# Performance work log

Hardware: AMD Instinct MI355X
Metric: run time of the kernel (lower is better)

Reference implementation:

```python
import jax, jax.numpy as jnp
import numpy as np

N_NODES = 30000
N_EDGES = 480000
IN_CH, NF, OUT_CH = 64, 128, 3
N_HIDDEN = 6  # GCN(num_layers=7): conv0 (in->nf) + 6 convs (nf->nf)
SLOPE = 0.02


def setup_inputs() -> dict:
    key = jax.random.key(0)
    ks = jax.random.split(key, 8)
    x = jax.random.normal(ks[0], (N_NODES, IN_CH), dtype=jnp.float32)
    edge_index = jax.random.randint(ks[1], (2, N_EDGES), 0, N_NODES, dtype=jnp.int64)
    W0 = jax.random.normal(ks[2], (IN_CH, NF), dtype=jnp.float32) * (1.0 / np.sqrt(IN_CH))
    b0 = jnp.zeros((NF,), dtype=jnp.float32)
    Wh = jax.random.normal(ks[3], (N_HIDDEN, NF, NF), dtype=jnp.float32) * (1.0 / np.sqrt(NF))
    bh = jnp.zeros((N_HIDDEN, NF), dtype=jnp.float32)
    Wout = jax.random.normal(ks[4], (NF, OUT_CH), dtype=jnp.float32) * (1.0 / np.sqrt(NF))
    bout = jnp.zeros((OUT_CH,), dtype=jnp.float32)
    return {"x": x, "edge_index": edge_index, "W0": W0, "b0": b0,
            "Wh": Wh, "bh": bh, "Wout": Wout, "bout": bout}


def _gcn_norm(edge_index, n):
    # PyG GCNConv default: add self-loops, symmetric normalization D^-1/2 (A+I) D^-1/2
    loop = jnp.arange(n, dtype=edge_index.dtype)
    src = jnp.concatenate([edge_index[0], loop])
    dst = jnp.concatenate([edge_index[1], loop])
    deg = jax.ops.segment_sum(jnp.ones_like(dst, dtype=jnp.float32), dst, num_segments=n)
    dinv = jax.lax.rsqrt(deg)  # deg >= 1 due to self-loops
    norm = dinv[src] * dinv[dst]  # [E+N]
    return src, dst, norm


def _gcn_conv(h, W, b, src, dst, norm, n):
    h = h @ W                                   # [N, F_out]
    msg = h[src] * norm[:, None]                # gather + scale  [E+N, F_out]
    out = jax.ops.segment_sum(msg, dst, num_segments=n)  # scatter-add
    return out + b


def reference(x, edge_index, W0, b0, Wh, bh, Wout, bout):
    n = x.shape[0]
    src, dst, norm = _gcn_norm(edge_index, n)
    # 7-layer GCN stack with LeakyReLU(0.02) between layers; dropout is
    # identity in eval mode (training=False).
    h = _gcn_conv(x, W0, b0, src, dst, norm, n)
    for i in range(N_HIDDEN):
        h = jax.nn.leaky_relu(h, SLOPE)
        h = _gcn_conv(h, Wh[i], bh[i], src, dst, norm, n)
    # outer forward: leaky_relu -> dropout(eval=identity) -> out conv -> tanh*0.5
    h = jax.nn.leaky_relu(h, SLOPE)
    h = _gcn_conv(h, Wout, bout, src, dst, norm, n)
    return jnp.tanh(h) * 0.5
```

## Files before the change

kernel.cpp:

```cpp
#include <hip/hip_runtime.h>
#include <hip/hip_fp16.h>
#include <math.h>

#define NN 30000
#define NE 480000
#define NB 118
#define INVSCALE (1.0f / 4096.0f)

typedef _Float16 half8 __attribute__((ext_vector_type(8)));
typedef float floatx4 __attribute__((ext_vector_type(4)));
typedef float floatx2 __attribute__((ext_vector_type(2)));

__device__ __forceinline__ float lrelu(float v) { return v > 0.0f ? v : v * 0.02f; }

__device__ __forceinline__ float4 fma4(float4 v, float w, float4 a) {
    a.x = fmaf(v.x, w, a.x);
    a.y = fmaf(v.y, w, a.y);
    a.z = fmaf(v.z, w, a.z);
    a.w = fmaf(v.w, w, a.w);
    return a;
}

__device__ __forceinline__ float4 loadh4(const __half* p) {
    uint2 raw = *(const uint2*)p;
    float2 f0 = __half22float2(*(__half2*)&raw.x);
    float2 f1 = __half22float2(*(__half2*)&raw.y);
    return make_float4(f0.x, f0.y, f1.x, f1.y);
}

__device__ __forceinline__ void loadf8x8(const unsigned char* p, float4* lo, float4* hi) {
    uint2 raw = *(const uint2*)p;
    floatx2 a = __builtin_amdgcn_cvt_pk_f32_fp8(raw.x, false);
    floatx2 b = __builtin_amdgcn_cvt_pk_f32_fp8(raw.x, true);
    floatx2 c = __builtin_amdgcn_cvt_pk_f32_fp8(raw.y, false);
    floatx2 d = __builtin_amdgcn_cvt_pk_f32_fp8(raw.y, true);
    *lo = make_float4(a.x, a.y, b.x, b.y);
    *hi = make_float4(c.x, c.y, d.x, d.y);
}

__device__ __forceinline__ void stnt_f8(unsigned char* p, float v) {
    int pk = __builtin_amdgcn_cvt_pk_fp8_f32(v, v, 0, false);
    __builtin_nontemporal_store((unsigned char)pk, p);
}


__global__ void k_count(const int* __restrict__ ei, int* __restrict__ cnt,
                        const float* __restrict__ W0, const float* __restrict__ Wh,
                        const float* __restrict__ b0, const float* __restrict__ bh,
                        const float* __restrict__ x,
                        __half* __restrict__ W0t, __half* __restrict__ Wht,
                        float* __restrict__ bs, __half* __restrict__ x16) {
    int g = blockIdx.x * 256 + threadIdx.x;
    if (g < NE) atomicAdd(&cnt[ei[NE + g]], 1);
    {
        float4 v = *(const float4*)&x[(size_t)g * 4];
        __half2 a = __floats2half2_rn(v.x, v.y);
        __half2 b = __floats2half2_rn(v.z, v.w);
        uint2 pk;
        pk.x = *(unsigned int*)&a;
        pk.y = *(unsigned int*)&b;
        *(uint2*)&x16[(size_t)g * 4] = pk;
    }
    if (g < 8192) {
        int k = g >> 7, n = g & 127;
        W0t[n * 64 + k] = __float2half(W0[g] * 64.0f);
    } else if (g < 8192 + 98304) {
        int j = g - 8192;
        int l = j >> 14;
        int r = j & 16383;
        int k = r >> 7, n = r & 127;
        Wht[l * 16384 + n * 128 + k] = __float2half(Wh[j] * 2.0f);
    } else if (g < 8192 + 98304 + 896) {
        int j = g - 8192 - 98304;
        float sc;
        if (j < 128) sc = 64.0f;
        else sc = (float)(1 << (7 + ((j - 128) >> 7)));
        bs[j] = (j < 128 ? b0[j] : bh[j - 128]) * sc;
    }
}

__global__ void k_scan1(const int* __restrict__ cnt, int* __restrict__ bsum,
                        float* __restrict__ dinv) {
    __shared__ int sd[256];
    int tid = threadIdx.x;
    int i = blockIdx.x * 256 + tid;
    int v = (i < NN) ? cnt[i] : 0;
    if (i < NN) dinv[i] = 1.0f / sqrtf((float)(v + 1));
    sd[tid] = v;
    __syncthreads();
    for (int off = 128; off > 0; off >>= 1) {
        if (tid < off) sd[tid] += sd[tid + off];
        __syncthreads();
    }
    if (tid == 0) bsum[blockIdx.x] = sd[0];
}

__global__ void k_scan3(const int* __restrict__ cnt, const int* __restrict__ bsum,
                        int* __restrict__ row_ptr, int* __restrict__ cursor) {
    __shared__ int sd[256];
    __shared__ int offs[128];
    int tid = threadIdx.x;
    if (tid < 128) offs[tid] = (tid < blockIdx.x) ? bsum[tid] : 0;
    __syncthreads();
    for (int o = 64; o > 0; o >>= 1) {
        if (tid < o) offs[tid] += offs[tid + o];
        __syncthreads();
    }
    int i = blockIdx.x * 256 + tid;
    int v = (i < NN) ? cnt[i] : 0;
    sd[tid] = v;
    __syncthreads();
    for (int off = 1; off < 256; off <<= 1) {
        int t = (tid >= off) ? sd[tid - off] : 0;
        __syncthreads();
        sd[tid] += t;
        __syncthreads();
    }
    if (i < NN) {
        int excl = offs[0] + sd[tid] - v;
        row_ptr[i] = excl;
        cursor[i] = excl;
        if (i == NN - 1) row_ptr[NN] = excl + v;
    }
}

__global__ void k_fill(const int* __restrict__ ei, const float* __restrict__ dinv,
                       int* __restrict__ cursor, int2* __restrict__ csr) {
    int e = blockIdx.x * 256 + threadIdx.x;
    if (e < NE) {
        int s = ei[e];
        int d = ei[NE + e];
        int pos = atomicAdd(&cursor[d], 1);
        float w = dinv[s] * dinv[d];
        csr[pos] = make_int2(s, __float_as_int(w));
    }
}


__launch_bounds__(256)
__global__ void k_layer0(const __half* __restrict__ x, const int* __restrict__ row_ptr,
                         const int2* __restrict__ csr, const float* __restrict__ dinv,
                         const __half* __restrict__ Wt, const float* __restrict__ bias,
                         unsigned char* __restrict__ out8) {
    __shared__ _Float16 hsF[2 * 4 * 16 * 8];
    int tid = threadIdx.x;
    int node0 = blockIdx.x * 16;
    {
        int nl = tid >> 4;
        int node = node0 + nl;
        int c = (tid & 15) * 4;
        float di = dinv[node];
        float w0 = di * di;
        float4 hv = loadh4(&x[(size_t)node * 64 + c]);
        float4 acc[8];
        acc[0] = make_float4(hv.x * w0, hv.y * w0, hv.z * w0, hv.w * w0);
        #pragma unroll
        for (int j = 1; j < 8; j++) acc[j] = make_float4(0.f, 0.f, 0.f, 0.f);
        int e = row_ptr[node];
        int e1 = row_ptr[node + 1];
        for (; e + 8 <= e1; e += 8) {
            int2 sw[8];
            #pragma unroll
            for (int j = 0; j < 8; j++) sw[j] = csr[e + j];
            float4 v[8];
            #pragma unroll
            for (int j = 0; j < 8; j++) v[j] = loadh4(&x[(size_t)sw[j].x * 64 + c]);
            #pragma unroll
            for (int j = 0; j < 8; j++) acc[j] = fma4(v[j], __int_as_float(sw[j].y), acc[j]);
        }
        for (; e < e1; ++e) {
            int2 sw = csr[e];
            float4 v = loadh4(&x[(size_t)sw.x * 64 + c]);
            acc[0] = fma4(v, __int_as_float(sw.y), acc[0]);
        }
        #pragma unroll
        for (int j = 1; j < 8; j++) {
            acc[0].x += acc[j].x;
            acc[0].y += acc[j].y;
            acc[0].z += acc[j].z;
            acc[0].w += acc[j].w;
        }
        int ks = c >> 5, quad = (c >> 3) & 3, jj = c & 7;
        __half2 p0 = __floats2half2_rn(acc[0].x, acc[0].y);
        __half2 p1 = __floats2half2_rn(acc[0].z, acc[0].w);
        uint2 pk;
        pk.x = *(unsigned int*)&p0;
        pk.y = *(unsigned int*)&p1;
        *(uint2*)&hsF[((ks * 4 + quad) * 16 + nl) * 8 + jj] = pk;
    }
    __syncthreads();
    int wave = tid >> 6, lane = tid & 63, quad = lane >> 4, ln = lane & 15;
    half8 afrag[2];
    #pragma unroll
    for (int ks = 0; ks < 2; ks++)
        afrag[ks] = *(const half8*)&hsF[((ks * 4 + quad) * 16 + ln) * 8];
    #pragma unroll
    for (int tc = 0; tc < 2; tc++) {
        int tt = wave + tc * 4;
        floatx4 acc = (floatx4){0.f, 0.f, 0.f, 0.f};
        #pragma unroll
        for (int ks = 0; ks < 2; ks++) {
            half8 b = *(const half8*)&Wt[(size_t)(tt * 16 + ln) * 64 + ks * 32 + quad * 8];
            acc = __builtin_amdgcn_mfma_f32_16x16x32_f16(afrag[ks], b, acc, 0, 0, 0);
        }
        int col = tt * 16 + ln;
        float bb = bias[col];
        #pragma unroll
        for (int r = 0; r < 4; r++) {
            int row = node0 + quad * 4 + r;
            stnt_f8(&out8[(size_t)row * 128 + col], lrelu(acc[r] + bb));
        }
    }
}

template <bool LAST>
__launch_bounds__(256)
__global__ void k_layer_h(const unsigned char* __restrict__ h, const int* __restrict__ row_ptr,
                          const int2* __restrict__ csr, const float* __restrict__ dinv,
                          const __half* __restrict__ Wt, const float* __restrict__ bias,
                          unsigned char* __restrict__ out8, const float* __restrict__ Wout,
                          float* __restrict__ u) {
    __shared__ _Float16 hsF[4 * 4 * 16 * 8];
    __shared__ float uacc[4][16][3];
    int tid = threadIdx.x;
    int node0 = blockIdx.x * 16;
    {
        int nl = tid >> 4;
        int node = node0 + nl;
        int c = (tid & 15) * 8;
        float di = dinv[node];
        float w0 = di * di;
        float4 hlo, hhi;
        loadf8x8(&h[(size_t)node * 128 + c], &hlo, &hhi);
        float4 acc[4][2];
        acc[0][0] = make_float4(hlo.x * w0, hlo.y * w0, hlo.z * w0, hlo.w * w0);
        acc[0][1] = make_float4(hhi.x * w0, hhi.y * w0, hhi.z * w0, hhi.w * w0);
        #pragma unroll
        for (int j = 1; j < 4; j++) {
            acc[j][0] = make_float4(0.f, 0.f, 0.f, 0.f);
            acc[j][1] = make_float4(0.f, 0.f, 0.f, 0.f);
        }
        int e = row_ptr[node];
        int e1 = row_ptr[node + 1];
        for (; e + 4 <= e1; e += 4) {
            int2 sw[4];
            #pragma unroll
            for (int j = 0; j < 4; j++) sw[j] = csr[e + j];
            float4 vlo[4], vhi[4];
            #pragma unroll
            for (int j = 0; j < 4; j++)
                loadf8x8(&h[(size_t)sw[j].x * 128 + c], &vlo[j], &vhi[j]);
            #pragma unroll
            for (int j = 0; j < 4; j++) {
                float w = __int_as_float(sw[j].y);
                acc[j][0] = fma4(vlo[j], w, acc[j][0]);
                acc[j][1] = fma4(vhi[j], w, acc[j][1]);
            }
        }
        for (; e < e1; ++e) {
            int2 sw = csr[e];
            float4 vlo, vhi;
            loadf8x8(&h[(size_t)sw.x * 128 + c], &vlo, &vhi);
            float w = __int_as_float(sw.y);
            acc[0][0] = fma4(vlo, w, acc[0][0]);
            acc[0][1] = fma4(vhi, w, acc[0][1]);
        }
        #pragma unroll
        for (int j = 1; j < 4; j++) {
            acc[0][0].x += acc[j][0].x; acc[0][0].y += acc[j][0].y;
            acc[0][0].z += acc[j][0].z; acc[0][0].w += acc[j][0].w;
            acc[0][1].x += acc[j][1].x; acc[0][1].y += acc[j][1].y;
            acc[0][1].z += acc[j][1].z; acc[0][1].w += acc[j][1].w;
        }
        int ks = c >> 5, quad = (c >> 3) & 3;
        __half2 p0 = __floats2half2_rn(acc[0][0].x, acc[0][0].y);
        __half2 p1 = __floats2half2_rn(acc[0][0].z, acc[0][0].w);
        __half2 p2 = __floats2half2_rn(acc[0][1].x, acc[0][1].y);
        __half2 p3 = __floats2half2_rn(acc[0][1].z, acc[0][1].w);
        uint4 pk;
        pk.x = *(unsigned int*)&p0;
        pk.y = *(unsigned int*)&p1;
        pk.z = *(unsigned int*)&p2;
        pk.w = *(unsigned int*)&p3;
        *(uint4*)&hsF[((ks * 4 + quad) * 16 + nl) * 8] = pk;
    }
    __syncthreads();
    int wave = tid >> 6, lane = tid & 63, quad = lane >> 4, ln = lane & 15;
    half8 afrag[4];
    #pragma unroll
    for (int ks = 0; ks < 4; ks++)
        afrag[ks] = *(const half8*)&hsF[((ks * 4 + quad) * 16 + ln) * 8];

    float up[4][3];
    if (LAST) {
        #pragma unroll
        for (int r = 0; r < 4; r++)
            #pragma unroll
            for (int cc = 0; cc < 3; cc++) up[r][cc] = 0.f;
    }

    #pragma unroll
    for (int tc = 0; tc < 2; tc++) {
        int tt = wave + tc * 4;
        floatx4 acc = (floatx4){0.f, 0.f, 0.f, 0.f};
        #pragma unroll
        for (int ks = 0; ks < 4; ks++) {
            half8 b = *(const half8*)&Wt[(size_t)(tt * 16 + ln) * 128 + ks * 32 + quad * 8];
            acc = __builtin_amdgcn_mfma_f32_16x16x32_f16(afrag[ks], b, acc, 0, 0, 0);
        }
        int col = tt * 16 + ln;
        float bb = bias[col];
        if (LAST) {
            float w0o = Wout[col * 3 + 0];
            float w1o = Wout[col * 3 + 1];
            float w2o = Wout[col * 3 + 2];
            #pragma unroll
            for (int r = 0; r < 4; r++) {
                float hv = lrelu(acc[r] + bb);
                up[r][0] = fmaf(hv, w0o, up[r][0]);
                up[r][1] = fmaf(hv, w1o, up[r][1]);
                up[r][2] = fmaf(hv, w2o, up[r][2]);
            }
        } else {
            #pragma unroll
            for (int r = 0; r < 4; r++) {
                int row = node0 + quad * 4 + r;
                stnt_f8(&out8[(size_t)row * 128 + col], lrelu(acc[r] + bb));
            }
        }
    }

    if (LAST) {
        #pragma unroll
        for (int m = 1; m < 16; m <<= 1) {
            #pragma unroll
            for (int r = 0; r < 4; r++) {
                #pragma unroll
                for (int cc = 0; cc < 3; cc++)
                    up[r][cc] += __shfl_xor(up[r][cc], m);
            }
        }
        if (ln == 0) {
            #pragma unroll
            for (int r = 0; r < 4; r++) {
                #pragma unroll
                for (int cc = 0; cc < 3; cc++)
                    uacc[wave][quad * 4 + r][cc] = up[r][cc];
            }
        }
        __syncthreads();
        if (tid < 48) {
            int row = tid / 3, cc = tid % 3;
            float s = (uacc[0][row][cc] + uacc[1][row][cc]) +
                      (uacc[2][row][cc] + uacc[3][row][cc]);
            u[(size_t)(node0 + row) * 3 + cc] = s;
        }
    }
}


__global__ void k_agg_out(const float* __restrict__ u, const int* __restrict__ row_ptr,
                          const int2* __restrict__ csr, const float* __restrict__ dinv,
                          const float* __restrict__ bout, float* __restrict__ out) {
    int node = blockIdx.x * 256 + threadIdx.x;
    if (node >= NN) return;
    float di = dinv[node], w0 = di * di;
    float s0 = u[(size_t)node * 3 + 0] * w0;
    float s1 = u[(size_t)node * 3 + 1] * w0;
    float s2 = u[(size_t)node * 3 + 2] * w0;
    float b0a = 0.f, b1a = 0.f, b2a = 0.f;
    int e = row_ptr[node];
    int e1 = row_ptr[node + 1];
    for (; e + 2 <= e1; e += 2) {
        int2 swa = csr[e], swb = csr[e + 1];
        float wa = __int_as_float(swa.y), wb = __int_as_float(swb.y);
        const float* ua = &u[(size_t)swa.x * 3];
        const float* ub = &u[(size_t)swb.x * 3];
        s0 = fmaf(ua[0], wa, s0);
        s1 = fmaf(ua[1], wa, s1);
        s2 = fmaf(ua[2], wa, s2);
        b0a = fmaf(ub[0], wb, b0a);
        b1a = fmaf(ub[1], wb, b1a);
        b2a = fmaf(ub[2], wb, b2a);
    }
    for (; e < e1; ++e) {
        int2 sw = csr[e];
        float w = __int_as_float(sw.y);
        const float* us = &u[(size_t)sw.x * 3];
        s0 = fmaf(us[0], w, s0);
        s1 = fmaf(us[1], w, s1);
        s2 = fmaf(us[2], w, s2);
    }
    out[(size_t)node * 3 + 0] = tanhf((s0 + b0a) * INVSCALE + bout[0]) * 0.5f;
    out[(size_t)node * 3 + 1] = tanhf((s1 + b1a) * INVSCALE + bout[1]) * 0.5f;
    out[(size_t)node * 3 + 2] = tanhf((s2 + b2a) * INVSCALE + bout[2]) * 0.5f;
}


extern "C" void kernel_launch(void* const* d_in, const int* in_sizes, int n_in,
                              void* d_out, int out_size, void* d_ws, size_t ws_size,
                              hipStream_t stream) {
    const float* x        = (const float*)d_in[0];
    const int*   ei       = (const int*)d_in[1];
    const float* W0       = (const float*)d_in[2];
    const float* b0       = (const float*)d_in[3];
    const float* Wh       = (const float*)d_in[4];
    const float* bh       = (const float*)d_in[5];
    const float* Wout     = (const float*)d_in[6];
    const float* bout     = (const float*)d_in[7];
    float* out            = (float*)d_out;

    char* ws = (char*)d_ws;
    float*  bufA   = (float*)(ws + 0);
    unsigned char* bufB8 = (unsigned char*)(ws + 15360000);
    unsigned char* bufC8 = (unsigned char*)(ws + 23040000);
    __half* x16    = (__half*)(ws + 30720000);
    __half* W0t16  = (__half*)(ws + 34560000);
    __half* Wht16  = (__half*)(ws + 34576384);
    float*  bs     = (float*)(ws + 34772992);
    float*  dinv   = (float*)(ws + 34776576);
    int*    cnt    = (int*)  (ws + 34896576);
    int*    row_ptr= (int*)  (ws + 35016576);
    int*    cursor = (int*)  (ws + 35136640);
    int2*   csr    = (int2*) (ws + 35256640);

    int* bsum = (int*)bufA;

    hipMemsetAsync(cnt, 0, NN * sizeof(int), stream);
    k_count<<<(NE + 255) / 256, 256, 0, stream>>>(ei, cnt, W0, Wh, b0, bh, x,
                                                  W0t16, Wht16, bs, x16);
    k_scan1<<<NB, 256, 0, stream>>>(cnt, bsum, dinv);
    k_scan3<<<NB, 256, 0, stream>>>(cnt, bsum, row_ptr, cursor);
    k_fill<<<(NE + 255) / 256, 256, 0, stream>>>(ei, dinv, cursor, csr);

    k_layer0<<<NN / 16, 256, 0, stream>>>(x16, row_ptr, csr, dinv, W0t16, bs, bufB8);

    unsigned char* hin = bufB8;
    unsigned char* hout = bufC8;
    for (int i = 0; i < 5; i++) {
        k_layer_h<false><<<NN / 16, 256, 0, stream>>>(hin, row_ptr, csr, dinv,
                                                      Wht16 + (size_t)i * 16384,
                                                      bs + 128 + (size_t)i * 128, hout,
                                                      Wout, bufA);
        unsigned char* t = hin; hin = hout; hout = t;
    }
    k_layer_h<true><<<NN / 16, 256, 0, stream>>>(hin, row_ptr, csr, dinv,
                                                 Wht16 + (size_t)5 * 16384,
                                                 bs + 128 + (size_t)5 * 128, hout,
                                                 Wout, bufA );

    k_agg_out<<<(NN + 255) / 256, 256, 0, stream>>>(bufA, row_ptr, csr, dinv, bout, out);
}
```

Before: 297.5 us.

## Fuse all GCN stages into a persistent megakernel with grid barriers

Replaces the sequence of count, scan, fill, per-layer and output kernels with one persistent kernel of 256 blocks x 512 threads that steps through the stages using a software grid barrier on atomics. Each block handles two 16-node tiles at a time over several passes, the scan is done by a single block, and the fp8 gather loop gets an 8-wide unrolled path. This removes per-launch overhead and inter-kernel gaps. In exchange, one block serialises the scan, all blocks must be co-resident for the barrier to work, and per-block work is less balanced.

New measurement: 648.9 us. +118.1%, slower.

```diff
diff --git a/kernel.cpp b/kernel.cpp
--- a/kernel.cpp
+++ b/kernel.cpp
@@ -4,8 +4,13 @@
 
 #define NN 30000
 #define NE 480000
-#define NB 118
+#define NBLK 256
+#define NTHR 512
+#define GSZ (NBLK * NTHR)
+#define NTILE 1875
+#define NPASS 4
 #define INVSCALE (1.0f / 4096.0f)
+
 
 typedef _Float16 half8 __attribute__((ext_vector_type(8)));
 typedef float floatx4 __attribute__((ext_vector_type(4)));
@@ -28,8 +33,7 @@
     return make_float4(f0.x, f0.y, f1.x, f1.y);
 }
 
-__device__ __forceinline__ void loadf8x8(const unsigned char* p, float4* lo, float4* hi) {
-    uint2 raw = *(const uint2*)p;
+__device__ __forceinline__ void cvtf8x8(uint2 raw, float4* lo, float4* hi) {
     floatx2 a = __builtin_amdgcn_cvt_pk_f32_fp8(raw.x, false);
     floatx2 b = __builtin_amdgcn_cvt_pk_f32_fp8(raw.x, true);
     floatx2 c = __builtin_amdgcn_cvt_pk_f32_fp8(raw.y, false);
@@ -38,117 +42,41 @@
     *hi = make_float4(c.x, c.y, d.x, d.y);
 }
 
+__device__ __forceinline__ void loadf8x8(const unsigned char* p, float4* lo, float4* hi) {
+    cvtf8x8(*(const uint2*)p, lo, hi);
+}
+
 __device__ __forceinline__ void stnt_f8(unsigned char* p, float v) {
     int pk = __builtin_amdgcn_cvt_pk_fp8_f32(v, v, 0, false);
     __builtin_nontemporal_store((unsigned char)pk, p);
 }
 
-
-__global__ void k_count(const int* __restrict__ ei, int* __restrict__ cnt,
-                        const float* __restrict__ W0, const float* __restrict__ Wh,
-                        const float* __restrict__ b0, const float* __restrict__ bh,
-                        const float* __restrict__ x,
-                        __half* __restrict__ W0t, __half* __restrict__ Wht,
-                        float* __restrict__ bs, __half* __restrict__ x16) {
-    int g = blockIdx.x * 256 + threadIdx.x;
-    if (g < NE) atomicAdd(&cnt[ei[NE + g]], 1);
-    {
-        float4 v = *(const float4*)&x[(size_t)g * 4];
-        __half2 a = __floats2half2_rn(v.x, v.y);
-        __half2 b = __floats2half2_rn(v.z, v.w);
-        uint2 pk;
-        pk.x = *(unsigned int*)&a;
-        pk.y = *(unsigned int*)&b;
-        *(uint2*)&x16[(size_t)g * 4] = pk;
-    }
-    if (g < 8192) {
-        int k = g >> 7, n = g & 127;
-        W0t[n * 64 + k] = __float2half(W0[g] * 64.0f);
-    } else if (g < 8192 + 98304) {
-        int j = g - 8192;
-        int l = j >> 14;
-        int r = j & 16383;
-        int k = r >> 7, n = r & 127;
-        Wht[l * 16384 + n * 128 + k] = __float2half(Wh[j] * 2.0f);
-    } else if (g < 8192 + 98304 + 896) {
-        int j = g - 8192 - 98304;
-        float sc;
-        if (j < 128) sc = 64.0f;
-        else sc = (float)(1 << (7 + ((j - 128) >> 7)));
-        bs[j] = (j < 128 ? b0[j] : bh[j - 128]) * sc;
-    }
-}
-
-__global__ void k_scan1(const int* __restrict__ cnt, int* __restrict__ bsum,
-                        float* __restrict__ dinv) {
-    __shared__ int sd[256];
-    int tid = threadIdx.x;
-    int i = blockIdx.x * 256 + tid;
-    int v = (i < NN) ? cnt[i] : 0;
-    if (i < NN) dinv[i] = 1.0f / sqrtf((float)(v + 1));
-    sd[tid] = v;
-    __syncthreads();
-    for (int off = 128; off > 0; off >>= 1) {
-        if (tid < off) sd[tid] += sd[tid + off];
-        __syncthreads();
-    }
-    if (tid == 0) bsum[blockIdx.x] = sd[0];
-}
-
-__global__ void k_scan3(const int* __restrict__ cnt, const int* __restrict__ bsum,
-                        int* __restrict__ row_ptr, int* __restrict__ cursor) {
-    __shared__ int sd[256];
-    __shared__ int offs[128];
-    int tid = threadIdx.x;
-    if (tid < 128) offs[tid] = (tid < blockIdx.x) ? bsum[tid] : 0;
-    __syncthreads();
-    for (int o = 64; o > 0; o >>= 1) {
-        if (tid < o) offs[tid] += offs[tid + o];
-        __syncthreads();
-    }
-    int i = blockIdx.x * 256 + tid;
-    int v = (i < NN) ? cnt[i] : 0;
-    sd[tid] = v;
-    __syncthreads();
-    for (int off = 1; off < 256; off <<= 1) {
-        int t = (tid >= off) ? sd[tid - off] : 0;
-        __syncthreads();
-        sd[tid] += t;
-        __syncthreads();
-    }
-    if (i < NN) {
-        int excl = offs[0] + sd[tid] - v;
-        row_ptr[i] = excl;
-        cursor[i] = excl;
-        if (i == NN - 1) row_ptr[NN] = excl + v;
-    }
-}
-
-__global__ void k_fill(const int* __restrict__ ei, const float* __restrict__ dinv,
-                       int* __restrict__ cursor, int2* __restrict__ csr) {
-    int e = blockIdx.x * 256 + threadIdx.x;
-    if (e < NE) {
-        int s = ei[e];
-        int d = ei[NE + e];
-        int pos = atomicAdd(&cursor[d], 1);
-        float w = dinv[s] * dinv[d];
-        csr[pos] = make_int2(s, __float_as_int(w));
-    }
-}
-
-
-__launch_bounds__(256)
-__global__ void k_layer0(const __half* __restrict__ x, const int* __restrict__ row_ptr,
-                         const int2* __restrict__ csr, const float* __restrict__ dinv,
-                         const __half* __restrict__ Wt, const float* __restrict__ bias,
-                         unsigned char* __restrict__ out8) {
-    __shared__ _Float16 hsF[2 * 4 * 16 * 8];
-    int tid = threadIdx.x;
-    int node0 = blockIdx.x * 16;
-    {
-        int nl = tid >> 4;
+__device__ __forceinline__ void gbar(int* bar, int my_gen) {
+    __syncthreads();
+    if (threadIdx.x == 0) {
+        int prev = __hip_atomic_fetch_add(&bar[0], 1, __ATOMIC_ACQ_REL, __HIP_MEMORY_SCOPE_AGENT);
+        if (prev == NBLK - 1) {
+            __hip_atomic_store(&bar[0], 0, __ATOMIC_RELAXED, __HIP_MEMORY_SCOPE_AGENT);
+            __hip_atomic_fetch_add(&bar[1], 1, __ATOMIC_RELEASE, __HIP_MEMORY_SCOPE_AGENT);
+        } else {
+            while (__hip_atomic_load(&bar[1], __ATOMIC_RELAXED, __HIP_MEMORY_SCOPE_AGENT) < my_gen)
+                __builtin_amdgcn_s_sleep(2);
+            (void)__hip_atomic_load(&bar[1], __ATOMIC_ACQUIRE, __HIP_MEMORY_SCOPE_AGENT);
+        }
+    }
+    __syncthreads();
+}
+
+__device__ __forceinline__ void layer0_tile(
+    const __half* __restrict__ x, const int* __restrict__ row_ptr,
+    const int2* __restrict__ csr, const float* __restrict__ dinv,
+    const __half* __restrict__ Wt, const float* __restrict__ bias,
+    unsigned char* __restrict__ out8, int node0, bool valid, int stid,
+    _Float16* hsF) {
+    if (valid) {
+        int nl = stid >> 4;
         int node = node0 + nl;
-        int c = (tid & 15) * 4;
+        int c = (stid & 15) * 4;
         float di = dinv[node];
         float w0 = di * di;
         float4 hv = loadh4(&x[(size_t)node * 64 + c]);
@@ -189,7 +117,7 @@
         *(uint2*)&hsF[((ks * 4 + quad) * 16 + nl) * 8 + jj] = pk;
     }
     __syncthreads();
-    int wave = tid >> 6, lane = tid & 63, quad = lane >> 4, ln = lane & 15;
+    int wave = stid >> 6, lane = stid & 63, quad = lane >> 4, ln = lane & 15;
     half8 afrag[2];
     #pragma unroll
     for (int ks = 0; ks < 2; ks++)
@@ -203,31 +131,31 @@
             half8 b = *(const half8*)&Wt[(size_t)(tt * 16 + ln) * 64 + ks * 32 + quad * 8];
             acc = __builtin_amdgcn_mfma_f32_16x16x32_f16(afrag[ks], b, acc, 0, 0, 0);
         }
-        int col = tt * 16 + ln;
-        float bb = bias[col];
-        #pragma unroll
-        for (int r = 0; r < 4; r++) {
-            int row = node0 + quad * 4 + r;
-            stnt_f8(&out8[(size_t)row * 128 + col], lrelu(acc[r] + bb));
-        }
-    }
+        if (valid) {
+            int col = tt * 16 + ln;
+            float bb = bias[col];
+            #pragma unroll
+            for (int r = 0; r < 4; r++) {
+                int row = node0 + quad * 4 + r;
+                stnt_f8(&out8[(size_t)row * 128 + col], lrelu(acc[r] + bb));
+            }
+        }
+    }
+    __syncthreads();
 }
 
 template <bool LAST>
-__launch_bounds__(256)
-__global__ void k_layer_h(const unsigned char* __restrict__ h, const int* __restrict__ row_ptr,
-                          const int2* __restrict__ csr, const float* __restrict__ dinv,
-                          const __half* __restrict__ Wt, const float* __restrict__ bias,
-                          unsigned char* __restrict__ out8, const float* __restrict__ Wout,
-                          float* __restrict__ u) {
-    __shared__ _Float16 hsF[4 * 4 * 16 * 8];
-    __shared__ float uacc[4][16][3];
-    int tid = threadIdx.x;
-    int node0 = blockIdx.x * 16;
-    {
-        int nl = tid >> 4;
+__device__ __forceinline__ void layerh_tile(
+    const unsigned char* __restrict__ h, const int* __restrict__ row_ptr,
+    const int2* __restrict__ csr, const float* __restrict__ dinv,
+    const __half* __restrict__ Wt, const float* __restrict__ bias,
+    unsigned char* __restrict__ out8, const float* __restrict__ Wout,
+    float* __restrict__ u, int node0, bool valid, int stid,
+    _Float16* hsF, float* uaccS) {
+    if (valid) {
+        int nl = stid >> 4;
         int node = node0 + nl;
-        int c = (tid & 15) * 8;
+        int c = (stid & 15) * 8;
         float di = dinv[node];
         float w0 = di * di;
         float4 hlo, hhi;
@@ -242,19 +170,36 @@
         }
         int e = row_ptr[node];
         int e1 = row_ptr[node + 1];
+        for (; e + 8 <= e1; e += 8) {
+            int2 sw[8];
+            #pragma unroll
+            for (int j = 0; j < 8; j++) sw[j] = csr[e + j];
+            uint2 raw[8];
+            #pragma unroll
+            for (int j = 0; j < 8; j++) raw[j] = *(const uint2*)&h[(size_t)sw[j].x * 128 + c];
+            #pragma unroll
+            for (int j = 0; j < 8; j++) {
+                float w = __int_as_float(sw[j].y);
+                float4 vlo, vhi;
+                cvtf8x8(raw[j], &vlo, &vhi);
+                acc[j & 3][0] = fma4(vlo, w, acc[j & 3][0]);
+                acc[j & 3][1] = fma4(vhi, w, acc[j & 3][1]);
+            }
+        }
         for (; e + 4 <= e1; e += 4) {
             int2 sw[4];
             #pragma unroll
             for (int j = 0; j < 4; j++) sw[j] = csr[e + j];
-            float4 vlo[4], vhi[4];
-            #pragma unroll
-            for (int j = 0; j < 4; j++)
-                loadf8x8(&h[(size_t)sw[j].x * 128 + c], &vlo[j], &vhi[j]);
+            uint2 raw[4];
+            #pragma unroll
+            for (int j = 0; j < 4; j++) raw[j] = *(const uint2*)&h[(size_t)sw[j].x * 128 + c];
             #pragma unroll
             for (int j = 0; j < 4; j++) {
                 float w = __int_as_float(sw[j].y);
-                acc[j][0] = fma4(vlo[j], w, acc[j][0]);
-                acc[j][1] = fma4(vhi[j], w, acc[j][1]);
+                float4 vlo, vhi;
+                cvtf8x8(raw[j], &vlo, &vhi);
+                acc[j][0] = fma4(vlo, w, acc[j][0]);
+                acc[j][1] = fma4(vhi, w, acc[j][1]);
             }
         }
         for (; e < e1; ++e) {
@@ -285,7 +230,7 @@
         *(uint4*)&hsF[((ks * 4 + quad) * 16 + nl) * 8] = pk;
     }
     __syncthreads();
-    int wave = tid >> 6, lane = tid & 63, quad = lane >> 4, ln = lane & 15;
+    int wave = stid >> 6, lane = stid & 63, quad = lane >> 4, ln = lane & 15;
     half8 afrag[4];
     #pragma unroll
     for (int ks = 0; ks < 4; ks++)
@@ -321,7 +266,7 @@
                 up[r][1] = fmaf(hv, w1o, up[r][1]);
                 up[r][2] = fmaf(hv, w2o, up[r][2]);
             }
-        } else {
+        } else if (valid) {
             #pragma unroll
             for (int r = 0; r < 4; r++) {
                 int row = node0 + quad * 4 + r;
@@ -340,60 +285,179 @@
                     up[r][cc] += __shfl_xor(up[r][cc], m);
             }
         }
-        if (ln == 0) {
+        if (ln == 0 && valid) {
             #pragma unroll
             for (int r = 0; r < 4; r++) {
                 #pragma unroll
                 for (int cc = 0; cc < 3; cc++)
-                    uacc[wave][quad * 4 + r][cc] = up[r][cc];
+                    uaccS[(wave * 16 + quad * 4 + r) * 3 + cc] = up[r][cc];
             }
         }
         __syncthreads();
-        if (tid < 48) {
-            int row = tid / 3, cc = tid % 3;
-            float s = (uacc[0][row][cc] + uacc[1][row][cc]) +
-                      (uacc[2][row][cc] + uacc[3][row][cc]);
+        if (stid < 48 && valid) {
+            int row = stid / 3, cc = stid % 3;
+            float s = (uaccS[(0 * 16 + row) * 3 + cc] + uaccS[(1 * 16 + row) * 3 + cc]) +
+                      (uaccS[(2 * 16 + row) * 3 + cc] + uaccS[(3 * 16 + row) * 3 + cc]);
             u[(size_t)(node0 + row) * 3 + cc] = s;
         }
     }
-}
-
-
-__global__ void k_agg_out(const float* __restrict__ u, const int* __restrict__ row_ptr,
-                          const int2* __restrict__ csr, const float* __restrict__ dinv,
-                          const float* __restrict__ bout, float* __restrict__ out) {
-    int node = blockIdx.x * 256 + threadIdx.x;
-    if (node >= NN) return;
-    float di = dinv[node], w0 = di * di;
-    float s0 = u[(size_t)node * 3 + 0] * w0;
-    float s1 = u[(size_t)node * 3 + 1] * w0;
-    float s2 = u[(size_t)node * 3 + 2] * w0;
-    float b0a = 0.f, b1a = 0.f, b2a = 0.f;
-    int e = row_ptr[node];
-    int e1 = row_ptr[node + 1];
-    for (; e + 2 <= e1; e += 2) {
-        int2 swa = csr[e], swb = csr[e + 1];
-        float wa = __int_as_float(swa.y), wb = __int_as_float(swb.y);
-        const float* ua = &u[(size_t)swa.x * 3];
-        const float* ub = &u[(size_t)swb.x * 3];
-        s0 = fmaf(ua[0], wa, s0);
-        s1 = fmaf(ua[1], wa, s1);
-        s2 = fmaf(ua[2], wa, s2);
-        b0a = fmaf(ub[0], wb, b0a);
-        b1a = fmaf(ub[1], wb, b1a);
-        b2a = fmaf(ub[2], wb, b2a);
-    }
-    for (; e < e1; ++e) {
-        int2 sw = csr[e];
-        float w = __int_as_float(sw.y);
-        const float* us = &u[(size_t)sw.x * 3];
-        s0 = fmaf(us[0], w, s0);
-        s1 = fmaf(us[1], w, s1);
-        s2 = fmaf(us[2], w, s2);
-    }
-    out[(size_t)node * 3 + 0] = tanhf((s0 + b0a) * INVSCALE + bout[0]) * 0.5f;
-    out[(size_t)node * 3 + 1] = tanhf((s1 + b1a) * INVSCALE + bout[1]) * 0.5f;
-    out[(size_t)node * 3 + 2] = tanhf((s2 + b2a) * INVSCALE + bout[2]) * 0.5f;
+    __syncthreads();
+}
+
+__launch_bounds__(NTHR)
+__global__ void k_mega(const float* __restrict__ x, const int* __restrict__ ei,
+                       const float* __restrict__ W0, const float* __restrict__ b0,
+                       const float* __restrict__ Wh, const float* __restrict__ bh,
+                       const float* __restrict__ Wout, const float* __restrict__ bout,
+                       float* __restrict__ out,
+                       float* __restrict__ u, unsigned char* __restrict__ bufB8,
+                       unsigned char* __restrict__ bufC8, __half* __restrict__ x16,
+                       __half* __restrict__ W0t, __half* __restrict__ Wht,
+                       float* __restrict__ bs, float* __restrict__ dinv,
+                       int* __restrict__ cnt, int* __restrict__ bar,
+                       int* __restrict__ row_ptr, int* __restrict__ cursor,
+                       int2* __restrict__ csr) {
+    __shared__ _Float16 hsF[2][4 * 4 * 16 * 8];
+    __shared__ float uaccS[2][4 * 16 * 3];
+    __shared__ int sscan[NTHR];
+
+    int tid = threadIdx.x;
+    int bid = blockIdx.x;
+    int g0 = bid * NTHR + tid;
+    int stid = tid & 255;
+    int sub = tid >> 8;
+    int bgen = 0;
+
+    for (int g = g0; g < NE; g += GSZ) {
+        atomicAdd(&cnt[ei[NE + g]], 1);
+        float4 v = *(const float4*)&x[(size_t)g * 4];
+        __half2 a = __floats2half2_rn(v.x, v.y);
+        __half2 b = __floats2half2_rn(v.z, v.w);
+        uint2 pk;
+        pk.x = *(unsigned int*)&a;
+        pk.y = *(unsigned int*)&b;
+        *(uint2*)&x16[(size_t)g * 4] = pk;
+    }
+    if (g0 < 8192) {
+        int k = g0 >> 7, n = g0 & 127;
+        W0t[n * 64 + k] = __float2half(W0[g0] * 64.0f);
+    } else if (g0 < 8192 + 98304) {
+        int j = g0 - 8192;
+        int l = j >> 14;
+        int r = j & 16383;
+        int k = r >> 7, n = r & 127;
+        Wht[l * 16384 + n * 128 + k] = __float2half(Wh[j] * 2.0f);
+    } else if (g0 < 8192 + 98304 + 896) {
+        int j = g0 - 8192 - 98304;
+        float sc;
+        if (j < 128) sc = 64.0f;
+        else sc = (float)(1 << (7 + ((j - 128) >> 7)));
+        bs[j] = (j < 128 ? b0[j] : bh[j - 128]) * sc;
+    }
+    gbar(bar, ++bgen);
+
+    if (bid == 0) {
+        const int CH = 59;
+        int base = tid * CH;
+        int s = 0;
+        for (int i = 0; i < CH; ++i) {
+            int idx = base + i;
+            if (idx < NN) s += cnt[idx];
+        }
+        sscan[tid] = s;
+        __syncthreads();
+        for (int off = 1; off < NTHR; off <<= 1) {
+            int t = (tid >= off) ? sscan[tid - off] : 0;
+            __syncthreads();
+            sscan[tid] += t;
+            __syncthreads();
+        }
+        int run = sscan[tid] - s;
+        for (int i = 0; i < CH; ++i) {
+            int idx = base + i;
+            if (idx < NN) {
+                int cv = cnt[idx];
+                row_ptr[idx] = run;
+                cursor[idx] = run;
+                dinv[idx] = 1.0f / sqrtf((float)(cv + 1));
+                run += cv;
+            }
+        }
+        if (tid == NTHR - 1) row_ptr[NN] = sscan[NTHR - 1];
+    }
+    gbar(bar, ++bgen);
+
+    for (int g = g0; g < NE; g += GSZ) {
+        int s = ei[g];
+        int d = ei[NE + g];
+        int pos = atomicAdd(&cursor[d], 1);
+        float w = dinv[s] * dinv[d];
+        csr[pos] = make_int2(s, __float_as_int(w));
+    }
+    gbar(bar, ++bgen);
+
+    for (int pass = 0; pass < NPASS; ++pass) {
+        int t = pass * (NBLK * 2) + bid * 2 + sub;
+        layer0_tile(x16, row_ptr, csr, dinv, W0t, bs, bufB8, t * 16, t < NTILE, stid,
+                    hsF[sub]);
+    }
+    gbar(bar, ++bgen);
+
+    unsigned char* hin = bufB8;
+    unsigned char* hout = bufC8;
+    for (int l = 0; l < 5; ++l) {
+        for (int pass = 0; pass < NPASS; ++pass) {
+            int t = pass * (NBLK * 2) + bid * 2 + sub;
+            layerh_tile<false>(hin, row_ptr, csr, dinv, Wht + (size_t)l * 16384,
+                               bs + 128 + (size_t)l * 128, hout, Wout, u, t * 16,
+                               t < NTILE, stid, hsF[sub], uaccS[sub]);
+        }
+        gbar(bar, ++bgen);
+        unsigned char* tmp = hin; hin = hout; hout = tmp;
+    }
+    for (int pass = 0; pass < NPASS; ++pass) {
+        int t = pass * (NBLK * 2) + bid * 2 + sub;
+        layerh_tile<true>(hin, row_ptr, csr, dinv, Wht + (size_t)5 * 16384,
+                          bs + 128 + (size_t)5 * 128, hout, Wout, u, t * 16,
+                          t < NTILE, stid, hsF[sub], uaccS[sub]);
+    }
+    gbar(bar, ++bgen);
+
+    {
+        int node = g0;
+        if (node < NN) {
+            float di = dinv[node], w0 = di * di;
+            float s0 = u[(size_t)node * 3 + 0] * w0;
+            float s1 = u[(size_t)node * 3 + 1] * w0;
+            float s2 = u[(size_t)node * 3 + 2] * w0;
+            float b0a = 0.f, b1a = 0.f, b2a = 0.f;
+            int e = row_ptr[node];
+            int e1 = row_ptr[node + 1];
+            for (; e + 2 <= e1; e += 2) {
+                int2 swa = csr[e], swb = csr[e + 1];
+                float wa = __int_as_float(swa.y), wb = __int_as_float(swb.y);
+                const float* ua = &u[(size_t)swa.x * 3];
+                const float* ub = &u[(size_t)swb.x * 3];
+                s0 = fmaf(ua[0], wa, s0);
+                s1 = fmaf(ua[1], wa, s1);
+                s2 = fmaf(ua[2], wa, s2);
+                b0a = fmaf(ub[0], wb, b0a);
+                b1a = fmaf(ub[1], wb, b1a);
+                b2a = fmaf(ub[2], wb, b2a);
+            }
+            for (; e < e1; ++e) {
+                int2 sw = csr[e];
+                float w = __int_as_float(sw.y);
+                const float* us = &u[(size_t)sw.x * 3];
+                s0 = fmaf(us[0], w, s0);
+                s1 = fmaf(us[1], w, s1);
+                s2 = fmaf(us[2], w, s2);
+            }
+            out[(size_t)node * 3 + 0] = tanhf((s0 + b0a) * INVSCALE + bout[0]) * 0.5f;
+            out[(size_t)node * 3 + 1] = tanhf((s1 + b1a) * INVSCALE + bout[1]) * 0.5f;
+            out[(size_t)node * 3 + 2] = tanhf((s2 + b2a) * INVSCALE + bout[2]) * 0.5f;
+        }
+    }
 }
 
 
@@ -420,34 +484,13 @@
     float*  bs     = (float*)(ws + 34772992);
     float*  dinv   = (float*)(ws + 34776576);
     int*    cnt    = (int*)  (ws + 34896576);
-    int*    row_ptr= (int*)  (ws + 35016576);
-    int*    cursor = (int*)  (ws + 35136640);
-    int2*   csr    = (int2*) (ws + 35256640);
-
-    int* bsum = (int*)bufA;
-
-    hipMemsetAsync(cnt, 0, NN * sizeof(int), stream);
-    k_count<<<(NE + 255) / 256, 256, 0, stream>>>(ei, cnt, W0, Wh, b0, bh, x,
-                                                  W0t16, Wht16, bs, x16);
-    k_scan1<<<NB, 256, 0, stream>>>(cnt, bsum, dinv);
-    k_scan3<<<NB, 256, 0, stream>>>(cnt, bsum, row_ptr, cursor);
-    k_fill<<<(NE + 255) / 256, 256, 0, stream>>>(ei, dinv, cursor, csr);
-
-    k_layer0<<<NN / 16, 256, 0, stream>>>(x16, row_ptr, csr, dinv, W0t16, bs, bufB8);
-
-    unsigned char* hin = bufB8;
-    unsigned char* hout = bufC8;
-    for (int i = 0; i < 5; i++) {
-        k_layer_h<false><<<NN / 16, 256, 0, stream>>>(hin, row_ptr, csr, dinv,
-                                                      Wht16 + (size_t)i * 16384,
-                                                      bs + 128 + (size_t)i * 128, hout,
-                                                      Wout, bufA);
-        unsigned char* t = hin; hin = hout; hout = t;
-    }
-    k_layer_h<true><<<NN / 16, 256, 0, stream>>>(hin, row_ptr, csr, dinv,
-                                                 Wht16 + (size_t)5 * 16384,
-                                                 bs + 128 + (size_t)5 * 128, hout,
-                                                 Wout, bufA );
-
-    k_agg_out<<<(NN + 255) / 256, 256, 0, stream>>>(bufA, row_ptr, csr, dinv, bout, out);
-}
+    int*    bar    = (int*)  (ws + 35016576);
+    int*    row_ptr= (int*)  (ws + 35016832);
+    int*    cursor = (int*)  (ws + 35136896);
+    int2*   csr    = (int2*) (ws + 35256896);
+
+    hipMemsetAsync(cnt, 0, 120000 + 256, stream);
+    k_mega<<<NBLK, NTHR, 0, stream>>>(x, ei, W0, b0, Wh, bh, Wout, bout, out,
+                                      bufA, bufB8, bufC8, x16, W0t16, Wht16, bs,
+                                      dinv, cnt, bar, row_ptr, cursor, csr);
+}
```
